# Kernel optimization log

Measured on AMD Instinct MI355X. Metric: run time of the kernel, lower is better.

The kernel has to match this reference:

```python
import jax, jax.numpy as jnp
import numpy as np

DIM = 192  # init dim; input channels = 2*DIM, output channels = DIM
EPS = 1e-5


def setup_inputs() -> dict:
    key = jax.random.key(0)
    k1, k2 = jax.random.split(key)
    x = jax.random.normal(k1, (2, 16, 32, 32, 2 * DIM), dtype=jnp.float32)
    W = jax.random.normal(k2, (2 * DIM, 8 * DIM), dtype=jnp.float32) * 0.02
    gamma = jnp.ones((2 * DIM,), dtype=jnp.float32)
    beta = jnp.zeros((2 * DIM,), dtype=jnp.float32)
    return {"x": x, "W": W, "gamma": gamma, "beta": beta}


def reference(x, W, gamma, beta):
    dim = DIM
    b, d, h, w, c = x.shape  # c == 2*dim
    # LayerNorm over last dim (biased variance, as torch)
    mu = jnp.mean(x, axis=-1, keepdims=True)
    var = jnp.var(x, axis=-1, keepdims=True)
    xn = (x - mu) * jax.lax.rsqrt(var + EPS) * gamma + beta
    # Linear expansion 2*dim -> 8*dim (no bias)
    xe = jnp.einsum('bdhwc,ce->bdhwe', xn, W)  # (b,d,h,w,8*dim)
    ch = lambda i: xe[..., i * dim:(i + 1) * dim]
    z = jnp.zeros((b, d, h, w, dim), dtype=xe.dtype)
    # Faithful to the torch code: parities (0,1,0) and (0,0,1) are written
    # are NEVER written (stay zero). Index = pd*4 + ph*2 + pw.
    grid = jnp.stack([
        ch(0), ch(6),  # (0,0,0), (0,0,1)
        ch(5), z,      # (0,1,0), (0,1,1)
        ch(1), ch(4),  # (1,0,0), (1,0,1)
        z,     ch(7),  # (1,1,0), (1,1,1)
    ], axis=4)  # (b,d,h,w,8,dim)
    grid = grid.reshape(b, d, h, w, 2, 2, 2, dim)
    # interleave parity axes: (b, d,pd, h,ph, w,pw, dim) -> (b,2d,2h,2w,dim)
    out = grid.transpose(0, 1, 4, 2, 5, 3, 6, 7).reshape(b, 2 * d, 2 * h, 2 * w, dim)
    return out
```

## Files before the change

### kernel.cpp

```cpp
#include <hip/hip_runtime.h>
#include <hip/hip_bf16.h>
#include <stdint.h>


typedef __attribute__((ext_vector_type(4))) float f32x4;
typedef __attribute__((ext_vector_type(8))) short s16x8;
typedef __attribute__((ext_vector_type(4))) unsigned short u16x4;
typedef const __attribute__((address_space(1))) void gvoid_t;
typedef __attribute__((address_space(3))) void lvoid_t;

__device__ __forceinline__ int ob_of_p(int p) {
    const int w = p & 31, h = (p >> 5) & 31, d = (p >> 10) & 15, b = p >> 14;
    return b * 25165824 + d * 1572864 + h * 24576 + w * 384;
}

__device__ __forceinline__ unsigned short f2bf(float f) {
    unsigned u = __builtin_bit_cast(unsigned, f);
    u += 0x7fffu + ((u >> 16) & 1u);
    return (unsigned short)(u >> 16);
}


__global__ __launch_bounds__(256) void lnwt_kernel(const float* __restrict__ x,
                                                   const float* __restrict__ gamma,
                                                   const float* __restrict__ beta,
                                                   const float* __restrict__ W,
                                                   float* __restrict__ outf,
                                                   unsigned short* __restrict__ xn,
                                                   unsigned short* __restrict__ wt) {
    if (blockIdx.x >= 8192) {
        const int t = (blockIdx.x - 8192) * 256 + threadIdx.x;
        const int k = t % 384;
        const int n = t / 384;
        const int s = n / 192;
        const int oc = (s < 2 ? s : s + 2) * 192 + (n % 192);
        wt[(size_t)n * 384 + k] = f2bf(W[(size_t)k * 1536 + oc]);
        return;
    }
    const int wv = threadIdx.x >> 6;
    const int l  = threadIdx.x & 63;
    const int p  = blockIdx.x * 4 + wv;
    const float* row = x + (size_t)p * 384;
    f32x4 v0 = *(const f32x4*)(row + l * 4);
    f32x4 v1 = {0.f, 0.f, 0.f, 0.f};
    if (l < 32) v1 = *(const f32x4*)(row + 256 + l * 4);
    float s  = v0[0]+v0[1]+v0[2]+v0[3] + v1[0]+v1[1]+v1[2]+v1[3];
    float s2 = v0[0]*v0[0]+v0[1]*v0[1]+v0[2]*v0[2]+v0[3]*v0[3]
             + v1[0]*v1[0]+v1[1]*v1[1]+v1[2]*v1[2]+v1[3]*v1[3];
    #pragma unroll
    for (int off = 32; off >= 1; off >>= 1) {
        s  += __shfl_xor(s,  off);
        s2 += __shfl_xor(s2, off);
    }
    const float mu = s * (1.f / 384.f);
    const float rs = rsqrtf(s2 * (1.f / 384.f) - mu * mu + 1e-5f);
    unsigned short* dst = xn + (size_t)p * 384;
    f32x4 g0 = *(const f32x4*)(gamma + l * 4);
    f32x4 b0 = *(const f32x4*)(beta  + l * 4);
    u16x4 o0;
    #pragma unroll
    for (int j = 0; j < 4; ++j) o0[j] = f2bf((v0[j] - mu) * rs * g0[j] + b0[j]);
    *(u16x4*)(dst + l * 4) = o0;
    if (l < 32) {
        f32x4 g1 = *(const f32x4*)(gamma + 256 + l * 4);
        f32x4 b1 = *(const f32x4*)(beta  + 256 + l * 4);
        u16x4 o1;
        #pragma unroll
        for (int j = 0; j < 4; ++j) o1[j] = f2bf((v1[j] - mu) * rs * g1[j] + b1[j]);
        *(u16x4*)(dst + 256 + l * 4) = o1;
    }
    if (l < 48) {
        const int ob = ob_of_p(p);
        const f32x4 z = {0.f, 0.f, 0.f, 0.f};
        *(f32x4*)(outf + ob + 12480  + l * 4) = z;
        *(f32x4*)(outf + ob + 798720 + l * 4) = z;
    }
}

__global__ __launch_bounds__(256) void gemm3_kernel(const unsigned short* __restrict__ xn,
                                                    const unsigned short* __restrict__ wt,
                                                    float* __restrict__ outf) {
    __shared__ char lds[65536];
    const char* xb = (const char*)xn;
    const char* wb = (const char*)wt;
    const int tid = threadIdx.x;
    const int wv = tid >> 6, l = tid & 63;
    int bid = blockIdx.x;
    bid = (bid & 7) * 288 + (bid >> 3);
    const int mt = bid / 9, nt = bid % 9;
    const int m0 = mt * 128, n0 = nt * 128;
    const int wm = wv >> 1, wn = wv & 1;

    size_t srcA[4], srcB[4];
    int ldsA[4], ldsB[4];
    #pragma unroll
    for (int i = 0; i < 4; ++i) {
        const int r = wv * 32 + i * 8 + (l >> 3);
        const int swz = ((l & 7) * 16) ^ ((r & 7) << 4);
        srcA[i] = (size_t)(m0 + r) * 768 + swz;
        srcB[i] = (size_t)(n0 + r) * 768 + swz;
        ldsA[i] = (wv * 32 + i * 8) * 128;
        ldsB[i] = 16384 + (wv * 32 + i * 8) * 128;
    }

    f32x4 acc[4][4];
    const f32x4 fz = {0.f, 0.f, 0.f, 0.f};
    #pragma unroll
    for (int m = 0; m < 4; ++m)
        #pragma unroll
        for (int n = 0; n < 4; ++n) acc[m][n] = fz;

    int arow[4], brow[4];
    #pragma unroll
    for (int i = 0; i < 4; ++i) {
        arow[i] = wm * 64 + i * 16 + (l & 15);
        brow[i] = wn * 64 + i * 16 + (l & 15);
    }
    const int kbyte0 = (l >> 4) * 16;

    #pragma unroll
    for (int i = 0; i < 4; ++i) {
        __builtin_amdgcn_global_load_lds((gvoid_t*)(xb + srcA[i]),
                                         (lvoid_t*)(lds + ldsA[i]), 16, 0, 0);
        __builtin_amdgcn_global_load_lds((gvoid_t*)(wb + srcB[i]),
                                         (lvoid_t*)(lds + ldsB[i]), 16, 0, 0);
    }
    __syncthreads();

    #pragma unroll
    for (int t = 0; t < 6; ++t) {
        const int cur = (t & 1) * 32768;
        const int nxt = 32768 - cur;
        if (t < 5) {
            #pragma unroll
            for (int i = 0; i < 4; ++i) {
                __builtin_amdgcn_global_load_lds((gvoid_t*)(xb + srcA[i] + (t + 1) * 128),
                                                 (lvoid_t*)(lds + nxt + ldsA[i]), 16, 0, 0);
                __builtin_amdgcn_global_load_lds((gvoid_t*)(wb + srcB[i] + (t + 1) * 128),
                                                 (lvoid_t*)(lds + nxt + ldsB[i]), 16, 0, 0);
            }
        }
        #pragma unroll
        for (int kk = 0; kk < 2; ++kk) {
            const int kbyte = kbyte0 + kk * 64;
            s16x8 a[4], b[4];
            #pragma unroll
            for (int m = 0; m < 4; ++m)
                a[m] = *(const s16x8*)(lds + cur + arow[m] * 128 + (kbyte ^ ((arow[m] & 7) << 4)));
            #pragma unroll
            for (int n = 0; n < 4; ++n)
                b[n] = *(const s16x8*)(lds + cur + 16384 + brow[n] * 128 + (kbyte ^ ((brow[n] & 7) << 4)));
            #pragma unroll
            for (int m = 0; m < 4; ++m)
                #pragma unroll
                for (int n = 0; n < 4; ++n)
                    acc[m][n] = __builtin_amdgcn_mfma_f32_16x16x32_bf16(a[m], b[n], acc[m][n], 0, 0, 0);
        }
        __syncthreads();
    }

    int coladd[4];
    #pragma unroll
    for (int n = 0; n < 4; ++n) {
        const int gnb = n0 + wn * 64 + n * 16;
        const int s = gnb / 192;
        int d;
        if      (s == 0) d = 0;
        else if (s == 1) d = 786432;
        else if (s == 2) d = 786624;
        else if (s == 3) d = 12288;
        else if (s == 4) d = 192;
        else             d = 798912;
        coladd[n] = d + (gnb % 192) + (l & 15);
    }
    const int pb = m0 + wm * 64 + (l >> 4) * 4;
    #pragma unroll
    for (int m = 0; m < 4; ++m) {
        #pragma unroll
        for (int r = 0; r < 4; ++r) {
            const int ob = ob_of_p(pb + m * 16 + r);
            #pragma unroll
            for (int n = 0; n < 4; ++n)
                outf[ob + coladd[n]] = acc[m][n][r];
        }
    }
}


__global__ __launch_bounds__(256) void ln_kernel(const float* __restrict__ x,
                                                 const float* __restrict__ gamma,
                                                 const float* __restrict__ beta,
                                                 float* __restrict__ outf) {
    const int wv = threadIdx.x >> 6;
    const int l  = threadIdx.x & 63;
    const int p  = blockIdx.x * 4 + wv;
    const float* row = x + (size_t)p * 384;
    f32x4 v0 = *(const f32x4*)(row + l * 4);
    f32x4 v1 = {0.f, 0.f, 0.f, 0.f};
    if (l < 32) v1 = *(const f32x4*)(row + 256 + l * 4);
    float s  = v0[0]+v0[1]+v0[2]+v0[3] + v1[0]+v1[1]+v1[2]+v1[3];
    float s2 = v0[0]*v0[0]+v0[1]*v0[1]+v0[2]*v0[2]+v0[3]*v0[3]
             + v1[0]*v1[0]+v1[1]*v1[1]+v1[2]*v1[2]+v1[3]*v1[3];
    #pragma unroll
    for (int off = 32; off >= 1; off >>= 1) {
        s  += __shfl_xor(s,  off);
        s2 += __shfl_xor(s2, off);
    }
    const float mu = s * (1.f / 384.f);
    const float rs = rsqrtf(s2 * (1.f / 384.f) - mu * mu + 1e-5f);
    unsigned short* dst = (unsigned short*)(outf + ob_of_p(p) + 12480);
    f32x4 g0 = *(const f32x4*)(gamma + l * 4);
    f32x4 b0 = *(const f32x4*)(beta  + l * 4);
    u16x4 o0;
    #pragma unroll
    for (int j = 0; j < 4; ++j) o0[j] = f2bf((v0[j] - mu) * rs * g0[j] + b0[j]);
    *(u16x4*)(dst + l * 4) = o0;
    if (l < 32) {
        f32x4 g1 = *(const f32x4*)(gamma + 256 + l * 4);
        f32x4 b1 = *(const f32x4*)(beta  + 256 + l * 4);
        u16x4 o1;
        #pragma unroll
        for (int j = 0; j < 4; ++j) o1[j] = f2bf((v1[j] - mu) * rs * g1[j] + b1[j]);
        *(u16x4*)(dst + 256 + l * 4) = o1;
    }
}

__global__ __launch_bounds__(256) void wt_kernel(const float* __restrict__ W,
                                                 float* __restrict__ outf) {
    const int t = blockIdx.x * 256 + threadIdx.x;
    const int k = t % 384;
    const int n = t / 384;
    const int s = n / 192;
    const int oc = (s < 2 ? s : s + 2) * 192 + (n % 192);
    const float v = W[(size_t)k * 1536 + oc];
    unsigned short* dst = (unsigned short*)(outf + ob_of_p(n) + 798720);
    dst[k] = f2bf(v);
}

__global__ __launch_bounds__(256) void gemm_kernel(float* __restrict__ outf) {
    __shared__ char lds[32768];
    const char* gbase = (const char*)outf;
    const int tid = threadIdx.x;
    const int wv = tid >> 6, l = tid & 63;
    int bid = blockIdx.x;
    bid = (bid & 7) * 288 + (bid >> 3);
    const int mt = bid / 9, nt = bid % 9;
    const int m0 = mt * 128, n0 = nt * 128;
    size_t srcA[4], srcB[4];
    int ldsA[4], ldsB[4];
    #pragma unroll
    for (int i = 0; i < 4; ++i) {
        const int r = wv * 32 + i * 8 + (l >> 3);
        const int swz = ((l & 7) * 16) ^ ((r & 7) << 4);
        srcA[i] = (size_t)(ob_of_p(m0 + r) + 12480)  * 4 + swz;
        srcB[i] = (size_t)(ob_of_p(n0 + r) + 798720) * 4 + swz;
        ldsA[i] = (wv * 32 + i * 8) * 128;
        ldsB[i] = 16384 + (wv * 32 + i * 8) * 128;
    }
    f32x4 acc[4][4];
    const f32x4 fz = {0.f, 0.f, 0.f, 0.f};
    #pragma unroll
    for (int m = 0; m < 4; ++m)
        #pragma unroll
        for (int n = 0; n < 4; ++n) acc[m][n] = fz;
    const int wm = wv >> 1, wn = wv & 1;
    int arow[4], brow[4];
    #pragma unroll
    for (int i = 0; i < 4; ++i) {
        arow[i] = wm * 64 + i * 16 + (l & 15);
        brow[i] = wn * 64 + i * 16 + (l & 15);
    }
    const int kbyte0 = (l >> 4) * 16;
    for (int t = 0; t < 6; ++t) {
        const int kb = t * 128;
        #pragma unroll
        for (int i = 0; i < 4; ++i)
            __builtin_amdgcn_global_load_lds((gvoid_t*)(gbase + srcA[i] + kb),
                                             (lvoid_t*)(lds + ldsA[i]), 16, 0, 0);
        #pragma unroll
        for (int i = 0; i < 4; ++i)
            __builtin_amdgcn_global_load_lds((gvoid_t*)(gbase + srcB[i] + kb),
                                             (lvoid_t*)(lds + ldsB[i]), 16, 0, 0);
        __syncthreads();
        #pragma unroll
        for (int kk = 0; kk < 2; ++kk) {
            const int kbyte = kbyte0 + kk * 64;
            s16x8 a[4], b[4];
            #pragma unroll
            for (int m = 0; m < 4; ++m)
                a[m] = *(const s16x8*)(lds + arow[m] * 128 + (kbyte ^ ((arow[m] & 7) << 4)));
            #pragma unroll
            for (int n = 0; n < 4; ++n)
                b[n] = *(const s16x8*)(lds + 16384 + brow[n] * 128 + (kbyte ^ ((brow[n] & 7) << 4)));
            #pragma unroll
            for (int m = 0; m < 4; ++m)
                #pragma unroll
                for (int n = 0; n < 4; ++n)
                    acc[m][n] = __builtin_amdgcn_mfma_f32_16x16x32_bf16(a[m], b[n], acc[m][n], 0, 0, 0);
        }
        __syncthreads();
    }
    int coladd[4];
    #pragma unroll
    for (int n = 0; n < 4; ++n) {
        const int gnb = n0 + wn * 64 + n * 16;
        const int s = gnb / 192;
        int d;
        if      (s == 0) d = 0;
        else if (s == 1) d = 786432;
        else if (s == 2) d = 786624;
        else if (s == 3) d = 12288;
        else if (s == 4) d = 192;
        else             d = 798912;
        coladd[n] = d + (gnb % 192) + (l & 15);
    }
    const int pb = m0 + wm * 64 + (l >> 4) * 4;
    #pragma unroll
    for (int m = 0; m < 4; ++m) {
        #pragma unroll
        for (int r = 0; r < 4; ++r) {
            const int ob = ob_of_p(pb + m * 16 + r);
            #pragma unroll
            for (int n = 0; n < 4; ++n)
                outf[ob + coladd[n]] = acc[m][n][r];
        }
    }
}

__global__ __launch_bounds__(256) void zero_kernel(float* __restrict__ outf) {
    const int idx = blockIdx.x * 256 + threadIdx.x;
    const int f4 = idx % 48;
    const int pr = (idx / 48) & 1;
    const int p  = idx / 96;
    const f32x4 z = {0.f, 0.f, 0.f, 0.f};
    *(f32x4*)(outf + ob_of_p(p) + (pr ? 798720 : 12480) + f4 * 4) = z;
}


extern "C" void kernel_launch(void* const* d_in, const int* in_sizes, int n_in,
                              void* d_out, int out_size, void* d_ws, size_t ws_size,
                              hipStream_t stream) {
    const float* x     = (const float*)d_in[0];
    const float* W     = (const float*)d_in[1];
    const float* gamma = (const float*)d_in[2];
    const float* beta  = (const float*)d_in[3];
    float* out = (float*)d_out;
    const size_t need = 25165824 + 884736;
    if (ws_size >= need) {
        unsigned short* xn = (unsigned short*)d_ws;
        unsigned short* wt = (unsigned short*)((char*)d_ws + 25165824);
        lnwt_kernel <<<9920, 256, 0, stream>>>(x, gamma, beta, W, out, xn, wt);
        gemm3_kernel<<<2304, 256, 0, stream>>>(xn, wt, out);
    } else {
        ln_kernel  <<<8192,  256, 0, stream>>>(x, gamma, beta, out);
        wt_kernel  <<<1728,  256, 0, stream>>>(W, out);
        gemm_kernel<<<2304,  256, 0, stream>>>(out);
        zero_kernel<<<12288, 256, 0, stream>>>(out);
    }
}
```

Before: 74.45 us.

## Fuse LayerNorm normalize into GEMM A-load, fold gamma/beta into weights and bias

The prep kernel now only computes per-row mean and rstd, and it folds gamma into the bf16 weight matrix and beta·W into a per-column bias. The GEMM loads fp32 x directly, applies the normalization, converts to bf16 and writes the result into swizzled LDS. This removes the 24 MB bf16 xn intermediate round trip. The zeroing of the never-written parity slots moves into the GEMM blocks with nt==0. The cost is that each A tile is reloaded as fp32 by all 9 N-tile blocks, doubling A read bytes, and register staging replaces the async global_load_lds for A.

```diff
diff --git a/kernel.cpp b/kernel.cpp
--- a/kernel.cpp
+++ b/kernel.cpp
@@ -5,6 +5,7 @@
 
 typedef __attribute__((ext_vector_type(4))) float f32x4;
 typedef __attribute__((ext_vector_type(8))) short s16x8;
+typedef __attribute__((ext_vector_type(4))) unsigned int u32x4;
 typedef __attribute__((ext_vector_type(4))) unsigned short u16x4;
 typedef const __attribute__((address_space(1))) void gvoid_t;
 typedef __attribute__((address_space(3))) void lvoid_t;
@@ -21,20 +22,34 @@
 }
 
 
-__global__ __launch_bounds__(256) void lnwt_kernel(const float* __restrict__ x,
+__global__ __launch_bounds__(256) void prep_kernel(const float* __restrict__ x,
                                                    const float* __restrict__ gamma,
                                                    const float* __restrict__ beta,
                                                    const float* __restrict__ W,
-                                                   float* __restrict__ outf,
-                                                   unsigned short* __restrict__ xn,
-                                                   unsigned short* __restrict__ wt) {
+                                                   float2* __restrict__ stats,
+                                                   unsigned short* __restrict__ wt,
+                                                   float* __restrict__ bias) {
     if (blockIdx.x >= 8192) {
-        const int t = (blockIdx.x - 8192) * 256 + threadIdx.x;
-        const int k = t % 384;
-        const int n = t / 384;
-        const int s = n / 192;
-        const int oc = (s < 2 ? s : s + 2) * 192 + (n % 192);
-        wt[(size_t)n * 384 + k] = f2bf(W[(size_t)k * 1536 + oc]);
+        const int xb = blockIdx.x - 8192;
+        if (xb < 1728) {
+            const int t = xb * 256 + threadIdx.x;
+            const int k = t % 384;
+            const int n = t / 384;
+            const int s = n / 192;
+            const int oc = (s < 2 ? s : s + 2) * 192 + (n % 192);
+            wt[(size_t)n * 384 + k] = f2bf(gamma[k] * W[(size_t)k * 1536 + oc]);
+        } else {
+            const int n = (xb - 1728) * 256 + threadIdx.x;
+            if (n < 1152) {
+                const int s = n / 192;
+                const int oc = (s < 2 ? s : s + 2) * 192 + (n % 192);
+                float a = 0.f;
+                #pragma unroll 4
+                for (int k = 0; k < 384; ++k)
+                    a = fmaf(beta[k], W[(size_t)k * 1536 + oc], a);
+                bias[n] = a;
+            }
+        }
         return;
     }
     const int wv = threadIdx.x >> 6;
@@ -54,34 +69,15 @@
     }
     const float mu = s * (1.f / 384.f);
     const float rs = rsqrtf(s2 * (1.f / 384.f) - mu * mu + 1e-5f);
-    unsigned short* dst = xn + (size_t)p * 384;
-    f32x4 g0 = *(const f32x4*)(gamma + l * 4);
-    f32x4 b0 = *(const f32x4*)(beta  + l * 4);
-    u16x4 o0;
-    #pragma unroll
-    for (int j = 0; j < 4; ++j) o0[j] = f2bf((v0[j] - mu) * rs * g0[j] + b0[j]);
-    *(u16x4*)(dst + l * 4) = o0;
-    if (l < 32) {
-        f32x4 g1 = *(const f32x4*)(gamma + 256 + l * 4);
-        f32x4 b1 = *(const f32x4*)(beta  + 256 + l * 4);
-        u16x4 o1;
-        #pragma unroll
-        for (int j = 0; j < 4; ++j) o1[j] = f2bf((v1[j] - mu) * rs * g1[j] + b1[j]);
-        *(u16x4*)(dst + 256 + l * 4) = o1;
-    }
-    if (l < 48) {
-        const int ob = ob_of_p(p);
-        const f32x4 z = {0.f, 0.f, 0.f, 0.f};
-        *(f32x4*)(outf + ob + 12480  + l * 4) = z;
-        *(f32x4*)(outf + ob + 798720 + l * 4) = z;
-    }
-}
-
-__global__ __launch_bounds__(256) void gemm3_kernel(const unsigned short* __restrict__ xn,
+    if (l == 0) stats[p] = make_float2(rs, -mu * rs);
+}
+
+__global__ __launch_bounds__(256) void gemm4_kernel(const float* __restrict__ x,
+                                                    const float2* __restrict__ stats,
                                                     const unsigned short* __restrict__ wt,
+                                                    const float* __restrict__ bias,
                                                     float* __restrict__ outf) {
     __shared__ char lds[65536];
-    const char* xb = (const char*)xn;
     const char* wb = (const char*)wt;
     const int tid = threadIdx.x;
     const int wv = tid >> 6, l = tid & 63;
@@ -91,15 +87,29 @@
     const int m0 = mt * 128, n0 = nt * 128;
     const int wm = wv >> 1, wn = wv & 1;
 
-    size_t srcA[4], srcB[4];
-    int ldsA[4], ldsB[4];
+    if (nt == 0) {
+        const int p  = m0 + (tid >> 1);
+        const int ob = ob_of_p(p) + ((tid & 1) ? 798720 : 12480);
+        const f32x4 z = {0.f, 0.f, 0.f, 0.f};
+        #pragma unroll
+        for (int j = 0; j < 12; ++j) *(f32x4*)(outf + ob + j * 4) = z;
+    }
+
+    const int ar = tid >> 1;
+    const int ah = tid & 1;
+    const float* asrc = x + (size_t)(m0 + ar) * 384 + ah * 32;
+    const float2 st = stats[m0 + ar];
+    const float rs = st.x, nmr = st.y;
+    int adst[4];
+    #pragma unroll
+    for (int j = 0; j < 4; ++j)
+        adst[j] = ar * 128 + (((ah * 4 + j) ^ (ar & 7)) << 4);
+
+    size_t srcB[4]; int ldsB[4];
     #pragma unroll
     for (int i = 0; i < 4; ++i) {
         const int r = wv * 32 + i * 8 + (l >> 3);
-        const int swz = ((l & 7) * 16) ^ ((r & 7) << 4);
-        srcA[i] = (size_t)(m0 + r) * 768 + swz;
-        srcB[i] = (size_t)(n0 + r) * 768 + swz;
-        ldsA[i] = (wv * 32 + i * 8) * 128;
+        srcB[i] = (size_t)(n0 + r) * 768 + (((l & 7) * 16) ^ ((r & 7) << 4));
         ldsB[i] = 16384 + (wv * 32 + i * 8) * 128;
     }
 
@@ -118,27 +128,41 @@
     }
     const int kbyte0 = (l >> 4) * 16;
 
-    #pragma unroll
-    for (int i = 0; i < 4; ++i) {
-        __builtin_amdgcn_global_load_lds((gvoid_t*)(xb + srcA[i]),
-                                         (lvoid_t*)(lds + ldsA[i]), 16, 0, 0);
-        __builtin_amdgcn_global_load_lds((gvoid_t*)(wb + srcB[i]),
-                                         (lvoid_t*)(lds + ldsB[i]), 16, 0, 0);
-    }
-    __syncthreads();
+    {
+        f32x4 av[8];
+        #pragma unroll
+        for (int q = 0; q < 8; ++q) av[q] = *(const f32x4*)(asrc + q * 4);
+        #pragma unroll
+        for (int i = 0; i < 4; ++i)
+            __builtin_amdgcn_global_load_lds((gvoid_t*)(wb + srcB[i]),
+                                             (lvoid_t*)(lds + ldsB[i]), 16, 0, 0);
+        #pragma unroll
+        for (int j = 0; j < 4; ++j) {
+            u32x4 c;
+            #pragma unroll
+            for (int w = 0; w < 4; ++w) {
+                const float f0 = fmaf(av[2 * j + (w >> 1)][(w & 1) * 2],     rs, nmr);
+                const float f1 = fmaf(av[2 * j + (w >> 1)][(w & 1) * 2 + 1], rs, nmr);
+                c[w] = (unsigned)f2bf(f0) | ((unsigned)f2bf(f1) << 16);
+            }
+            *(u32x4*)(lds + adst[j]) = c;
+        }
+        __syncthreads();
+    }
 
     #pragma unroll
     for (int t = 0; t < 6; ++t) {
         const int cur = (t & 1) * 32768;
         const int nxt = 32768 - cur;
+        f32x4 av[8];
         if (t < 5) {
             #pragma unroll
-            for (int i = 0; i < 4; ++i) {
-                __builtin_amdgcn_global_load_lds((gvoid_t*)(xb + srcA[i] + (t + 1) * 128),
-                                                 (lvoid_t*)(lds + nxt + ldsA[i]), 16, 0, 0);
+            for (int q = 0; q < 8; ++q)
+                av[q] = *(const f32x4*)(asrc + (t + 1) * 64 + q * 4);
+            #pragma unroll
+            for (int i = 0; i < 4; ++i)
                 __builtin_amdgcn_global_load_lds((gvoid_t*)(wb + srcB[i] + (t + 1) * 128),
                                                  (lvoid_t*)(lds + nxt + ldsB[i]), 16, 0, 0);
-            }
         }
         #pragma unroll
         for (int kk = 0; kk < 2; ++kk) {
@@ -156,10 +180,24 @@
                 for (int n = 0; n < 4; ++n)
                     acc[m][n] = __builtin_amdgcn_mfma_f32_16x16x32_bf16(a[m], b[n], acc[m][n], 0, 0, 0);
         }
+        if (t < 5) {
+            #pragma unroll
+            for (int j = 0; j < 4; ++j) {
+                u32x4 c;
+                #pragma unroll
+                for (int w = 0; w < 4; ++w) {
+                    const float f0 = fmaf(av[2 * j + (w >> 1)][(w & 1) * 2],     rs, nmr);
+                    const float f1 = fmaf(av[2 * j + (w >> 1)][(w & 1) * 2 + 1], rs, nmr);
+                    c[w] = (unsigned)f2bf(f0) | ((unsigned)f2bf(f1) << 16);
+                }
+                *(u32x4*)(lds + nxt + adst[j]) = c;
+            }
+        }
         __syncthreads();
     }
 
     int coladd[4];
+    float badd[4];
     #pragma unroll
     for (int n = 0; n < 4; ++n) {
         const int gnb = n0 + wn * 64 + n * 16;
@@ -172,6 +210,7 @@
         else if (s == 4) d = 192;
         else             d = 798912;
         coladd[n] = d + (gnb % 192) + (l & 15);
+        badd[n]   = bias[gnb + (l & 15)];
     }
     const int pb = m0 + wm * 64 + (l >> 4) * 4;
     #pragma unroll
@@ -181,7 +220,7 @@
             const int ob = ob_of_p(pb + m * 16 + r);
             #pragma unroll
             for (int n = 0; n < 4; ++n)
-                outf[ob + coladd[n]] = acc[m][n][r];
+                outf[ob + coladd[n]] = acc[m][n][r] + badd[n];
         }
     }
 }
@@ -345,12 +384,13 @@
     const float* gamma = (const float*)d_in[2];
     const float* beta  = (const float*)d_in[3];
     float* out = (float*)d_out;
-    const size_t need = 25165824 + 884736;
+    const size_t need = 262144 + 884736 + 4608;
     if (ws_size >= need) {
-        unsigned short* xn = (unsigned short*)d_ws;
-        unsigned short* wt = (unsigned short*)((char*)d_ws + 25165824);
-        lnwt_kernel <<<9920, 256, 0, stream>>>(x, gamma, beta, W, out, xn, wt);
-        gemm3_kernel<<<2304, 256, 0, stream>>>(xn, wt, out);
+        float2*         st = (float2*)d_ws;
+        unsigned short* wt = (unsigned short*)((char*)d_ws + 262144);
+        float*          bi = (float*)((char*)d_ws + 1146880);
+        prep_kernel <<<9925, 256, 0, stream>>>(x, gamma, beta, W, st, wt, bi);
+        gemm4_kernel<<<2304, 256, 0, stream>>>(x, st, wt, bi, out);
     } else {
         ln_kernel  <<<8192,  256, 0, stream>>>(x, gamma, beta, out);
         wt_kernel  <<<1728,  256, 0, stream>>>(W, out);
```

Measured after the change: 116.6 us. +56.6%, slower.
